# Kernel tuning notes

Hardware: AMD Instinct MI355X
Metric: run time of the kernel (lower is better)

Reference implementation:

```python
import jax, jax.numpy as jnp
import numpy as np

BATCH, SEQ, D_MODEL = 8, 2048, 512
HEADS, BUCKET, N_HASHES = 8, 4, 4
D_HEAD = D_MODEL // HEADS
N_BUCKETS = SEQ // BUCKET
SELF_ATTN_VAL = -5e4  # TOKEN_SELF_ATTN_VALUE in reformer-pytorch


def setup_inputs() -> dict:
    key = jax.random.key(0)
    ks = jax.random.split(key, 8)
    scale = 1.0 / np.sqrt(D_MODEL).astype(np.float32)
    q = jax.random.normal(ks[0], (BATCH, SEQ, D_MODEL), jnp.float32)
    k = jax.random.normal(ks[1], (BATCH, SEQ, D_MODEL), jnp.float32)
    v = jax.random.normal(ks[2], (BATCH, SEQ, D_MODEL), jnp.float32)
    Wqk = jax.random.normal(ks[3], (D_MODEL, D_MODEL), jnp.float32) * scale
    Wv = jax.random.normal(ks[4], (D_MODEL, D_MODEL), jnp.float32) * scale
    Wout = jax.random.normal(ks[5], (D_MODEL, D_MODEL), jnp.float32) * scale
    b_out = jnp.zeros((D_MODEL,), jnp.float32)
    rotations = jax.random.normal(ks[6], (D_HEAD, N_HASHES, N_BUCKETS // 2), jnp.float32)
    return {"queries": q, "keys": k, "values": v, "Wqk": Wqk, "Wv": Wv,
            "Wout": Wout, "b_out": b_out, "rotations": rotations}


def _look_one_back(x):
    # concat each chunk with the previous chunk (wrap-around), along within-chunk axis
    return jnp.concatenate([x, jnp.roll(x, 1, axis=1)], axis=2)


def _lsh_attend(qk, v, rotations, bucket_size, n_hashes):
    # qk, v: (bm, t, d); shared-QK LSH attention (reformer-pytorch defaults)
    bm, t, d = qk.shape
    n_buckets = t // bucket_size
    # --- hash ---
    rotated = jnp.einsum('btf,fhi->bhti', qk, rotations)          # (bm, nh, t, nb/2)
    rotated = jnp.concatenate([rotated, -rotated], axis=-1)       # (bm, nh, t, nb)
    buckets = jnp.argmax(rotated, axis=-1)                        # (bm, nh, t)
    offsets = (jnp.arange(n_hashes) * n_buckets)[None, :, None]
    buckets = (buckets + offsets).reshape(bm, n_hashes * t)
    # --- sort tokens by (bucket, position) ---
    ticker = jnp.arange(n_hashes * t)
    buckets_and_t = t * buckets + (ticker % t)[None, :]           # unique values
    sticker = jnp.argsort(buckets_and_t, axis=-1)                 # (bm, nh*t)
    undo_sort = jnp.argsort(sticker, axis=-1)
    st = sticker % t
    sqk = jnp.take_along_axis(qk, st[:, :, None], axis=1)         # (bm, nh*t, d)
    sv = jnp.take_along_axis(v, st[:, :, None], axis=1)
    # --- chunk ---
    n_chunks = n_hashes * n_buckets
    bq_t = st.reshape(bm, n_chunks, bucket_size)
    bqk = sqk.reshape(bm, n_chunks, bucket_size, d)
    bv = sv.reshape(bm, n_chunks, bucket_size, d)
    bq = bqk
    norm = jnp.maximum(jnp.linalg.norm(bqk, axis=-1, keepdims=True), 1e-12)
    bk = bqk / norm                                               # F.normalize (shared QK)
    bk = _look_one_back(bk)
    bv = _look_one_back(bv)
    bkv_t = jnp.concatenate([bq_t, jnp.roll(bq_t, 1, axis=1)], axis=2)
    # --- attend within chunks ---
    dots = jnp.einsum('bnie,bnje->bnij', bq, bk) * (d ** -0.5)    # (bm, nc, bs, 2bs)
    self_mask = bq_t[:, :, :, None] == bkv_t[:, :, None, :]
    dots = jnp.where(self_mask, SELF_ATTN_VAL, dots)
    dots_lse = jax.nn.logsumexp(dots, axis=-1, keepdims=True)
    probs = jnp.exp(dots - dots_lse)
    bo = jnp.einsum('bnij,bnje->bnie', probs, bv)
    so = bo.reshape(bm, -1, d)
    slogits = dots_lse.reshape(bm, -1)
    # --- unsort and combine hash rounds ---
    o = jnp.take_along_axis(so, undo_sort[:, :, None], axis=1)
    logits = jnp.take_along_axis(slogits, undo_sort, axis=1)
    o = o.reshape(bm, n_hashes, t, d)
    logits = logits.reshape(bm, n_hashes, t, 1)
    w = jnp.exp(logits - jax.nn.logsumexp(logits, axis=1, keepdims=True))
    return jnp.sum(o * w, axis=1)                                 # (bm, t, d)


def reference(queries, keys, values, Wqk, Wv, Wout, b_out, rotations):
    # keys/values are unused by the original module (self-attention on queries)
    B, N, C = queries.shape
    H, d = HEADS, C // HEADS
    qk = jnp.einsum('bnc,cd->bnd', queries, Wqk)
    v = jnp.einsum('bnc,cd->bnd', queries, Wv)
    qk = qk.reshape(B, N, H, d).transpose(0, 2, 1, 3).reshape(B * H, N, d)
    v = v.reshape(B, N, H, d).transpose(0, 2, 1, 3).reshape(B * H, N, d)
    o = _lsh_attend(qk, v, rotations, BUCKET, N_HASHES)
    o = o.reshape(B, H, N, d).transpose(0, 2, 1, 3).reshape(B, N, C)
    return jnp.einsum('bnc,cd->bnd', o, Wout) + b_out
```

## Files before the change

kernel.cpp:

```cpp
#include <hip/hip_runtime.h>
#include <math.h>

#define SELF_VAL (-5e4f)

typedef __attribute__((ext_vector_type(8))) short bf16x8;
typedef __attribute__((ext_vector_type(4))) float f32x4;

__device__ __forceinline__ unsigned short f2bf(float x) {
    unsigned b = __float_as_uint(x);
    b += 0x7FFFu + ((b >> 16) & 1u);
    return (unsigned short)(b >> 16);
}
__device__ __forceinline__ float bf2f(unsigned short h) {
    return __uint_as_float(((unsigned)h) << 16);
}

__global__ __launch_bounds__(256) void k_rotT(const float* __restrict__ rot,
                                              float* __restrict__ rotT2)
{
    int idx = blockIdx.x * 256 + threadIdx.x;
    int h = idx >> 14, k = (idx >> 8) & 63, col = idx & 255;
    rotT2[idx] = rot[k * 1024 + h * 256 + col];
}

__global__ __launch_bounds__(256) void k_woutT(const float* __restrict__ Wout,
                                               unsigned short* __restrict__ WoutT16)
{
    int idx = blockIdx.x * 256 + threadIdx.x;
    int n = idx >> 9, k = idx & 511;
    WoutT16[idx] = f2bf(Wout[(size_t)k * 512 + n]);
}

__global__ __launch_bounds__(256) void k_gemm_qkv(
    const float* __restrict__ Q, const float* __restrict__ Wqk,
    const float* __restrict__ Wv, float* __restrict__ qk, float* __restrict__ vv,
    float* __restrict__ rnorm)
{
    __shared__ float As[16][132];
    __shared__ float Bs[16][132];
    const int bx = blockIdx.x;
    const int mt = bx >> 3, nt = bx & 7;
    const int m0 = mt * 128, n0 = nt * 128;
    const int tid = threadIdx.x;
    const int ty = tid >> 4, tx = tid & 15;
    const float* Bsrc = (n0 < 512) ? (Wqk + n0) : (Wv + (n0 - 512));
    const int ar0 = tid >> 2, acq = (tid & 3) * 4;
    const int ar1 = 64 + (tid >> 2);
    const int bk0 = tid >> 5, bnq = (tid & 31) * 4;
    const int bk1 = 8 + (tid >> 5);
    const float* Aptr0 = Q + (size_t)(m0 + ar0) * 512 + acq;
    const float* Aptr1 = Q + (size_t)(m0 + ar1) * 512 + acq;
    const float* Bptr0 = Bsrc + (size_t)bk0 * 512 + bnq;
    const float* Bptr1 = Bsrc + (size_t)bk1 * 512 + bnq;
    float acc[8][8] = {};
    float4 a0 = *(const float4*)(Aptr0);
    float4 a1 = *(const float4*)(Aptr1);
    float4 b0 = *(const float4*)(Bptr0);
    float4 b1 = *(const float4*)(Bptr1);
    for (int k0 = 0; k0 < 512; k0 += 16) {
        As[acq+0][ar0]=a0.x; As[acq+1][ar0]=a0.y; As[acq+2][ar0]=a0.z; As[acq+3][ar0]=a0.w;
        As[acq+0][ar1]=a1.x; As[acq+1][ar1]=a1.y; As[acq+2][ar1]=a1.z; As[acq+3][ar1]=a1.w;
        *(float4*)&Bs[bk0][bnq] = b0;
        *(float4*)&Bs[bk1][bnq] = b1;
        __syncthreads();
        if (k0 + 16 < 512) {
            a0 = *(const float4*)(Aptr0 + k0 + 16);
            a1 = *(const float4*)(Aptr1 + k0 + 16);
            b0 = *(const float4*)(Bptr0 + (size_t)(k0 + 16) * 512);
            b1 = *(const float4*)(Bptr1 + (size_t)(k0 + 16) * 512);
        }
        #pragma unroll
        for (int kk = 0; kk < 16; kk++) {
            float a_[8], b_[8];
            *(float4*)&a_[0] = *(float4*)&As[kk][ty*4];
            *(float4*)&a_[4] = *(float4*)&As[kk][64 + ty*4];
            *(float4*)&b_[0] = *(float4*)&Bs[kk][tx*4];
            *(float4*)&b_[4] = *(float4*)&Bs[kk][64 + tx*4];
            #pragma unroll
            for (int i = 0; i < 8; i++)
                #pragma unroll
                for (int j = 0; j < 8; j++)
                    acc[i][j] += a_[i] * b_[j];
        }
        __syncthreads();
    }
    #pragma unroll
    for (int ig = 0; ig < 2; ig++) {
        #pragma unroll
        for (int i = 0; i < 4; i++) {
            int row = m0 + ig*64 + ty*4 + i;
            int b = row >> 11, t = row & 2047;
            #pragma unroll
            for (int jg = 0; jg < 2; jg++) {
                int n = n0 + jg*64 + tx*4;
                float4 r4 = make_float4(acc[ig*4+i][jg*4+0], acc[ig*4+i][jg*4+1],
                                        acc[ig*4+i][jg*4+2], acc[ig*4+i][jg*4+3]);
                if (n < 512) {
                    *(float4*)(qk + ((size_t)((b*8 + (n>>6))*2048 + t))*64 + (n&63)) = r4;
                } else {
                    int nv = n - 512;
                    *(float4*)(vv + ((size_t)((b*8 + (nv>>6))*2048 + t))*64 + (nv&63)) = r4;
                }
            }
        }
    }
    if (n0 < 512) {
        #pragma unroll
        for (int jg = 0; jg < 2; jg++) {
            int h = (n0 + jg*64) >> 6;
            #pragma unroll
            for (int ig = 0; ig < 2; ig++) {
                #pragma unroll
                for (int i = 0; i < 4; i++) {
                    float s = acc[ig*4+i][jg*4+0]*acc[ig*4+i][jg*4+0]
                            + acc[ig*4+i][jg*4+1]*acc[ig*4+i][jg*4+1]
                            + acc[ig*4+i][jg*4+2]*acc[ig*4+i][jg*4+2]
                            + acc[ig*4+i][jg*4+3]*acc[ig*4+i][jg*4+3];
                    s += __shfl_xor(s, 1);
                    s += __shfl_xor(s, 2);
                    s += __shfl_xor(s, 4);
                    s += __shfl_xor(s, 8);
                    if (tx == 0) {
                        int row = m0 + ig*64 + ty*4 + i;
                        int b = row >> 11, t = row & 2047;
                        rnorm[((size_t)(b*8 + h))*2048 + t] = 1.0f / fmaxf(sqrtf(s), 1e-12f);
                    }
                }
            }
        }
    }
}

__global__ __launch_bounds__(256) void k_hash(const float* __restrict__ qk,
    const float* __restrict__ rotT2, unsigned* __restrict__ buckets)
{
    __shared__ float As[64*128];
    const int bx = blockIdx.x;
    const int bm = bx >> 4;
    const int row0 = (bx & 15) << 7;
    const int tid = threadIdx.x;
    const int ty = tid >> 4, tx = tid & 15;
    {
        const int r = tid >> 1;
        const int kb = (tid & 1) * 8;
        const float* src = qk + ((size_t)(bm*2048 + row0 + r))*64;
        #pragma unroll
        for (int c = 0; c < 8; c++) {
            float4 a4 = *(const float4*)(src + (size_t)(kb + c)*4);
            int k = (kb + c)*4;
            As[(k+0)*128 + r] = a4.x;
            As[(k+1)*128 + r] = a4.y;
            As[(k+2)*128 + r] = a4.z;
            As[(k+3)*128 + r] = a4.w;
        }
    }
    __syncthreads();
    #pragma unroll 1
    for (int h = 0; h < 4; h++) {
        float bv[8]; unsigned bi[8];
        #pragma unroll
        for (int i = 0; i < 8; i++) { bv[i] = -3.402823466e38f; bi[i] = 0u; }
        #pragma unroll 1
        for (int ch = 0; ch < 4; ch++) {
            const float* bsrc = rotT2 + (size_t)h*16384 + ch*64 + tx*4;
            float acc[8][4] = {};
            #pragma unroll 16
            for (int kk = 0; kk < 64; kk++) {
                float4 b4 = *(const float4*)(bsrc + (size_t)kk*256);
                float a_[8];
                *(float4*)&a_[0] = *(float4*)&As[kk*128 + ty*4];
                *(float4*)&a_[4] = *(float4*)&As[kk*128 + 64 + ty*4];
                float b_[4] = {b4.x, b4.y, b4.z, b4.w};
                #pragma unroll
                for (int i = 0; i < 8; i++)
                    #pragma unroll
                    for (int j = 0; j < 4; j++)
                        acc[i][j] += a_[i] * b_[j];
            }
            #pragma unroll
            for (int j = 0; j < 4; j++) {
                unsigned c0 = (unsigned)(ch*64 + tx*4 + j);
                unsigned nc0 = 256u + c0;
                #pragma unroll
                for (int i = 0; i < 8; i++) {
                    float v = acc[i][j];
                    if (v > bv[i] || (v == bv[i] && c0 < bi[i])) { bv[i] = v; bi[i] = c0; }
                    float nv = -v;
                    if (nv > bv[i] || (nv == bv[i] && nc0 < bi[i])) { bv[i] = nv; bi[i] = nc0; }
                }
            }
        }
        #pragma unroll
        for (int i = 0; i < 8; i++) {
            #pragma unroll
            for (int d = 1; d < 16; d <<= 1) {
                float ov = __shfl_xor(bv[i], d);
                unsigned oi = (unsigned)__shfl_xor((int)bi[i], d);
                if (ov > bv[i] || (ov == bv[i] && oi < bi[i])) { bv[i] = ov; bi[i] = oi; }
            }
        }
        if (tx == 0) {
            #pragma unroll
            for (int i = 0; i < 8; i++) {
                int r = (i < 4) ? (ty*4 + i) : (64 + ty*4 + (i - 4));
                buckets[((size_t)(bm*4 + h))*2048 + row0 + r] = bi[i];
            }
        }
    }
}

__global__ __launch_bounds__(256) void k_sort(const unsigned* __restrict__ buckets,
                                              unsigned* __restrict__ st)
{
    __shared__ unsigned whist[4][512];
    __shared__ unsigned baseb[512];
    const int seg = blockIdx.x;
    const unsigned* bk = buckets + (size_t)seg * 2048;
    unsigned* out = st + (size_t)seg * 2048;
    const int tid = threadIdx.x, w = tid >> 6, lane = tid & 63;
    for (int b = tid; b < 2048; b += 256) ((unsigned*)whist)[b] = 0u;
    __syncthreads();
    unsigned myb[8];
    #pragma unroll
    for (int r = 0; r < 8; r++) {
        int pos = w*512 + r*64 + lane;
        myb[r] = bk[pos];
        atomicAdd(&whist[w][myb[r]], 1u);
    }
    __syncthreads();
    for (int b = tid; b < 512; b += 256) {
        unsigned p = 0;
        #pragma unroll
        for (int ww = 0; ww < 4; ww++) { unsigned t = whist[ww][b]; whist[ww][b] = p; p += t; }
        baseb[b] = p;
    }
    __syncthreads();
    if (tid == 0) {
        unsigned run = 0;
        for (int b = 0; b < 512; b++) { unsigned t = baseb[b]; baseb[b] = run; run += t; }
    }
    __syncthreads();
    for (int b = tid; b < 512; b += 256) {
        unsigned bb = baseb[b];
        #pragma unroll
        for (int ww = 0; ww < 4; ww++) whist[ww][b] += bb;
    }
    __syncthreads();
    for (int r = 0; r < 8; r++) {
        unsigned b = myb[r];
        int pos = w*512 + r*64 + lane;
        unsigned base = whist[w][b];
        unsigned rank = 0;
        for (int j = 0; j < 64; j++) {
            unsigned bj = __shfl(b, j);
            rank += (j < lane && bj == b) ? 1u : 0u;
        }
        out[base + rank] = (unsigned)pos;
        atomicAdd(&whist[w][b], 1u);
    }
}

__global__ __launch_bounds__(256) void k_attn(const float* __restrict__ qk,
    const float* __restrict__ vv, const float* __restrict__ rnorm,
    const unsigned* __restrict__ st, unsigned short* __restrict__ oh16,
    float* __restrict__ logits)
{
    __shared__ float qs[68][68];
    __shared__ float vs[68][68];
    __shared__ unsigned P[68];
    __shared__ float rn[68];
    const int sid = blockIdx.x;
    const int stripi = sid & 31;
    const int seg = sid >> 5;
    const int bm = seg >> 2, h = seg & 3;
    const int G0 = (h*512 + stripi*16) * 4;
    const int tid = threadIdx.x;
    for (int j = tid; j < 68; j += 256) {
        int G = (G0 - 4 + j) & 8191;
        int hg = G >> 11, sg = G & 2047;
        unsigned tok = st[((size_t)(bm*4 + hg))*2048 + sg];
        P[j] = tok;
        rn[j] = rnorm[bm*2048 + (int)tok];
    }
    __syncthreads();
    for (int e = tid; e < 68*16; e += 256) {
        int j = e >> 4, fq = e & 15;
        unsigned tok = P[j];
        size_t base = ((size_t)(bm*2048 + (int)tok))*64 + fq*4;
        *(float4*)&qs[j][fq*4] = *(const float4*)(qk + base);
        *(float4*)&vs[j][fq*4] = *(const float4*)(vv + base);
    }
    __syncthreads();
    const int w = tid >> 6, lane = tid & 63;
    const int half = lane >> 5, qi = (lane >> 3) & 3, jj = lane & 7;
    const int fb = lane & 7;
    for (int cp = 0; cp < 2; cp++) {
        int c = w*4 + cp*2 + half;
        int jq = 4 + c*4 + qi;
        int jk = c*4 + jj;
        float dot = 0.f;
        #pragma unroll
        for (int fq = 0; fq < 16; fq++) {
            float4 q4 = *(float4*)&qs[jq][fq*4];
            float4 k4 = *(float4*)&qs[jk][fq*4];
            dot += q4.x*k4.x + q4.y*k4.y + q4.z*k4.z + q4.w*k4.w;
        }
        dot *= 0.125f * rn[jk];
        if (P[jq] == P[jk]) dot = SELF_VAL;
        float m = dot;
        m = fmaxf(m, __shfl_xor(m, 1));
        m = fmaxf(m, __shfl_xor(m, 2));
        m = fmaxf(m, __shfl_xor(m, 4));
        float ex = expf(dot - m);
        float s = ex;
        s += __shfl_xor(s, 1); s += __shfl_xor(s, 2); s += __shfl_xor(s, 4);
        float lse = m + logf(s);
        float p = expf(dot - lse);
        unsigned tq = P[jq];
        if (jj == 0) logits[((size_t)(bm*4 + h))*2048 + tq] = lse;
        float a0=0,a1=0,a2=0,a3=0,a4a=0,a5=0,a6=0,a7=0;
        #pragma unroll
        for (int j2 = 0; j2 < 8; j2++) {
            float pj = __shfl(p, (lane & 0x38) | j2);
            float4 va = *(float4*)&vs[c*4 + j2][fb*8];
            float4 vb = *(float4*)&vs[c*4 + j2][fb*8 + 4];
            a0 += pj*va.x; a1 += pj*va.y; a2 += pj*va.z; a3 += pj*va.w;
            a4a += pj*vb.x; a5 += pj*vb.y; a6 += pj*vb.z; a7 += pj*vb.w;
        }
        union { unsigned short s[8]; uint4 v; } ob;
        ob.s[0]=f2bf(a0); ob.s[1]=f2bf(a1); ob.s[2]=f2bf(a2); ob.s[3]=f2bf(a3);
        ob.s[4]=f2bf(a4a); ob.s[5]=f2bf(a5); ob.s[6]=f2bf(a6); ob.s[7]=f2bf(a7);
        *(uint4*)(oh16 + ((size_t)((bm*4 + h)*2048 + (int)tq))*64 + fb*8) = ob.v;
    }
}

__global__ __launch_bounds__(256) void k_combine(const unsigned short* __restrict__ oh16,
    const float* __restrict__ logits, unsigned short* __restrict__ comb16)
{
    int w = threadIdx.x >> 6, lane = threadIdx.x & 63;
    int row = blockIdx.x * 4 + w;
    int bm = row >> 11, t = row & 2047;
    int b = bm >> 3, head = bm & 7;
    float l0 = logits[((size_t)(bm*4 + 0))*2048 + t];
    float l1 = logits[((size_t)(bm*4 + 1))*2048 + t];
    float l2 = logits[((size_t)(bm*4 + 2))*2048 + t];
    float l3 = logits[((size_t)(bm*4 + 3))*2048 + t];
    float m = fmaxf(fmaxf(l0, l1), fmaxf(l2, l3));
    float e0 = expf(l0 - m), e1 = expf(l1 - m), e2 = expf(l2 - m), e3 = expf(l3 - m);
    float inv = 1.0f / (e0 + e1 + e2 + e3);
    float o = 0.f;
    o += (e0*inv) * bf2f(oh16[((size_t)((bm*4+0)*2048 + t))*64 + lane]);
    o += (e1*inv) * bf2f(oh16[((size_t)((bm*4+1)*2048 + t))*64 + lane]);
    o += (e2*inv) * bf2f(oh16[((size_t)((bm*4+2)*2048 + t))*64 + lane]);
    o += (e3*inv) * bf2f(oh16[((size_t)((bm*4+3)*2048 + t))*64 + lane]);
    comb16[((size_t)(b*2048 + t))*512 + head*64 + lane] = f2bf(o);
}

__global__ __launch_bounds__(256) void k_gemm_out(
    const unsigned short* __restrict__ comb16, const unsigned short* __restrict__ WoutT16,
    const float* __restrict__ bias, float* __restrict__ out)
{
    __shared__ unsigned short Asl[64*72];
    __shared__ unsigned short Bsl[64*72];
    const int bx = blockIdx.x;
    const int mt = bx >> 3, nt = bx & 7;
    const int m0 = mt*64, n0 = nt*64;
    const int tid = threadIdx.x;
    const int wid = tid >> 6, lane = tid & 63;
    const int wm = wid >> 1, wn = wid & 1;
    const int l15 = lane & 15, l4 = lane >> 4;
    const int srow = tid >> 2, skb = (tid & 3) * 16;
    f32x4 acc[2][2] = {};
    for (int k0 = 0; k0 < 512; k0 += 64) {
        {
            const unsigned short* asrc = comb16 + (size_t)(m0 + srow)*512 + k0 + skb;
            *(uint4*)&Asl[srow*72 + skb]     = *(const uint4*)asrc;
            *(uint4*)&Asl[srow*72 + skb + 8] = *(const uint4*)(asrc + 8);
            const unsigned short* bsrc = WoutT16 + (size_t)(n0 + srow)*512 + k0 + skb;
            *(uint4*)&Bsl[srow*72 + skb]     = *(const uint4*)bsrc;
            *(uint4*)&Bsl[srow*72 + skb + 8] = *(const uint4*)(bsrc + 8);
        }
        __syncthreads();
        #pragma unroll
        for (int kq = 0; kq < 2; kq++) {
            int kb = kq*32 + l4*8;
            bf16x8 a0 = *(bf16x8*)&Asl[(wm*32 +      l15)*72 + kb];
            bf16x8 a1 = *(bf16x8*)&Asl[(wm*32 + 16 + l15)*72 + kb];
            bf16x8 b0 = *(bf16x8*)&Bsl[(wn*32 +      l15)*72 + kb];
            bf16x8 b1 = *(bf16x8*)&Bsl[(wn*32 + 16 + l15)*72 + kb];
            acc[0][0] = __builtin_amdgcn_mfma_f32_16x16x32_bf16(a0, b0, acc[0][0], 0, 0, 0);
            acc[0][1] = __builtin_amdgcn_mfma_f32_16x16x32_bf16(a0, b1, acc[0][1], 0, 0, 0);
            acc[1][0] = __builtin_amdgcn_mfma_f32_16x16x32_bf16(a1, b0, acc[1][0], 0, 0, 0);
            acc[1][1] = __builtin_amdgcn_mfma_f32_16x16x32_bf16(a1, b1, acc[1][1], 0, 0, 0);
        }
        __syncthreads();
    }
    #pragma unroll
    for (int sm = 0; sm < 2; sm++) {
        #pragma unroll
        for (int sn = 0; sn < 2; sn++) {
            int col = n0 + wn*32 + sn*16 + l15;
            float bb = bias[col];
            #pragma unroll
            for (int r = 0; r < 4; r++) {
                int row = m0 + wm*32 + sm*16 + l4*4 + r;
                out[(size_t)row*512 + col] = acc[sm][sn][r] + bb;
            }
        }
    }
}

extern "C" void kernel_launch(void* const* d_in, const int* in_sizes, int n_in,
                              void* d_out, int out_size, void* d_ws, size_t ws_size,
                              hipStream_t stream)
{
    const float* Q    = (const float*)d_in[0];
    const float* Wqk  = (const float*)d_in[3];
    const float* Wv   = (const float*)d_in[4];
    const float* Wout = (const float*)d_in[5];
    const float* bout = (const float*)d_in[6];
    const float* rot  = (const float*)d_in[7];
    float* ws = (float*)d_ws;
    float* qk     = ws;
    float* vv     = ws + 8388608;
    unsigned short* oh16 = (unsigned short*)(ws + 16777216);
    unsigned short* WoutT16 = (unsigned short*)(ws + 33554432);
    unsigned short* comb16  = (unsigned short*)(ws + 50331648);
    float* rnorm  = ws + 58720256;
    float* logits = ws + 58851328;
    unsigned* buckets = (unsigned*)(ws + 59375616);
    unsigned* st      = (unsigned*)(ws + 59899904);
    float* rotT2  = ws + 60424192;
    float* out = (float*)d_out;

    k_rotT    <<<dim3(256),  dim3(256), 0, stream>>>(rot, rotT2);
    k_woutT   <<<dim3(1024), dim3(256), 0, stream>>>(Wout, WoutT16);
    k_gemm_qkv<<<dim3(1024), dim3(256), 0, stream>>>(Q, Wqk, Wv, qk, vv, rnorm);
    k_hash    <<<dim3(1024), dim3(256), 0, stream>>>(qk, rotT2, buckets);
    k_sort    <<<dim3(256),  dim3(256), 0, stream>>>(buckets, st);
    k_attn    <<<dim3(8192), dim3(256), 0, stream>>>(qk, vv, rnorm, st, oh16, logits);
    k_combine <<<dim3(32768),dim3(256), 0, stream>>>(oh16, logits, comb16);
    k_gemm_out<<<dim3(2048), dim3(256), 0, stream>>>(comb16, WoutT16, bout, out);
}
```

Measured before the change: 619.3 us.

## Split QKV GEMM and compute V projection with bf16 MFMA

Splits the fused fp32 QK/V projection into two kernels. QK stays on the fp32 SIMT path, since it feeds hashing and norms that are sensitive to precision. V is computed with bf16 MFMA after converting Q and transposing Wv to bf16. This should cut the V half of the fp32 GEMM cost. In exchange it adds conversion kernels, extra memory traffic and bf16 rounding error in V.

```diff
diff --git a/kernel.cpp b/kernel.cpp
--- a/kernel.cpp
+++ b/kernel.cpp
@@ -31,19 +31,39 @@
     WoutT16[idx] = f2bf(Wout[(size_t)k * 512 + n]);
 }
 
-__global__ __launch_bounds__(256) void k_gemm_qkv(
+__global__ __launch_bounds__(256) void k_wvT(const float* __restrict__ Wv,
+                                             unsigned short* __restrict__ WvT16)
+{
+    int idx = blockIdx.x * 256 + threadIdx.x;
+    int n = idx >> 9, k = idx & 511;
+    WvT16[idx] = f2bf(Wv[(size_t)k * 512 + n]);
+}
+
+__global__ __launch_bounds__(256) void k_q16(const float* __restrict__ Q,
+                                             unsigned short* __restrict__ Q16)
+{
+    int idx = blockIdx.x * 256 + threadIdx.x;
+    const float* src = Q + (size_t)idx * 8;
+    float4 v0 = *(const float4*)src;
+    float4 v1 = *(const float4*)(src + 4);
+    union { unsigned short s[8]; uint4 v; } ob;
+    ob.s[0]=f2bf(v0.x); ob.s[1]=f2bf(v0.y); ob.s[2]=f2bf(v0.z); ob.s[3]=f2bf(v0.w);
+    ob.s[4]=f2bf(v1.x); ob.s[5]=f2bf(v1.y); ob.s[6]=f2bf(v1.z); ob.s[7]=f2bf(v1.w);
+    *(uint4*)(Q16 + (size_t)idx * 8) = ob.v;
+}
+
+__global__ __launch_bounds__(256) void k_gemm_qk(
     const float* __restrict__ Q, const float* __restrict__ Wqk,
-    const float* __restrict__ Wv, float* __restrict__ qk, float* __restrict__ vv,
-    float* __restrict__ rnorm)
+    float* __restrict__ qk, float* __restrict__ rnorm)
 {
     __shared__ float As[16][132];
     __shared__ float Bs[16][132];
     const int bx = blockIdx.x;
-    const int mt = bx >> 3, nt = bx & 7;
+    const int mt = bx >> 2, nt = bx & 3;
     const int m0 = mt * 128, n0 = nt * 128;
     const int tid = threadIdx.x;
     const int ty = tid >> 4, tx = tid & 15;
-    const float* Bsrc = (n0 < 512) ? (Wqk + n0) : (Wv + (n0 - 512));
+    const float* Bsrc = Wqk + n0;
     const int ar0 = tid >> 2, acq = (tid & 3) * 4;
     const int ar1 = 64 + (tid >> 2);
     const int bk0 = tid >> 5, bnq = (tid & 31) * 4;
@@ -95,37 +115,85 @@
                 int n = n0 + jg*64 + tx*4;
                 float4 r4 = make_float4(acc[ig*4+i][jg*4+0], acc[ig*4+i][jg*4+1],
                                         acc[ig*4+i][jg*4+2], acc[ig*4+i][jg*4+3]);
-                if (n < 512) {
-                    *(float4*)(qk + ((size_t)((b*8 + (n>>6))*2048 + t))*64 + (n&63)) = r4;
-                } else {
-                    int nv = n - 512;
-                    *(float4*)(vv + ((size_t)((b*8 + (nv>>6))*2048 + t))*64 + (nv&63)) = r4;
+                *(float4*)(qk + ((size_t)((b*8 + (n>>6))*2048 + t))*64 + (n&63)) = r4;
+            }
+        }
+    }
+    #pragma unroll
+    for (int jg = 0; jg < 2; jg++) {
+        int h = (n0 + jg*64) >> 6;
+        #pragma unroll
+        for (int ig = 0; ig < 2; ig++) {
+            #pragma unroll
+            for (int i = 0; i < 4; i++) {
+                float s = acc[ig*4+i][jg*4+0]*acc[ig*4+i][jg*4+0]
+                        + acc[ig*4+i][jg*4+1]*acc[ig*4+i][jg*4+1]
+                        + acc[ig*4+i][jg*4+2]*acc[ig*4+i][jg*4+2]
+                        + acc[ig*4+i][jg*4+3]*acc[ig*4+i][jg*4+3];
+                s += __shfl_xor(s, 1);
+                s += __shfl_xor(s, 2);
+                s += __shfl_xor(s, 4);
+                s += __shfl_xor(s, 8);
+                if (tx == 0) {
+                    int row = m0 + ig*64 + ty*4 + i;
+                    int b = row >> 11, t = row & 2047;
+                    rnorm[((size_t)(b*8 + h))*2048 + t] = 1.0f / fmaxf(sqrtf(s), 1e-12f);
                 }
             }
         }
     }
-    if (n0 < 512) {
-        #pragma unroll
-        for (int jg = 0; jg < 2; jg++) {
-            int h = (n0 + jg*64) >> 6;
-            #pragma unroll
-            for (int ig = 0; ig < 2; ig++) {
-                #pragma unroll
-                for (int i = 0; i < 4; i++) {
-                    float s = acc[ig*4+i][jg*4+0]*acc[ig*4+i][jg*4+0]
-                            + acc[ig*4+i][jg*4+1]*acc[ig*4+i][jg*4+1]
-                            + acc[ig*4+i][jg*4+2]*acc[ig*4+i][jg*4+2]
-                            + acc[ig*4+i][jg*4+3]*acc[ig*4+i][jg*4+3];
-                    s += __shfl_xor(s, 1);
-                    s += __shfl_xor(s, 2);
-                    s += __shfl_xor(s, 4);
-                    s += __shfl_xor(s, 8);
-                    if (tx == 0) {
-                        int row = m0 + ig*64 + ty*4 + i;
-                        int b = row >> 11, t = row & 2047;
-                        rnorm[((size_t)(b*8 + h))*2048 + t] = 1.0f / fmaxf(sqrtf(s), 1e-12f);
-                    }
-                }
+}
+
+__global__ __launch_bounds__(256) void k_gemm_v(
+    const unsigned short* __restrict__ Q16, const unsigned short* __restrict__ WvT16,
+    float* __restrict__ vv)
+{
+    __shared__ unsigned short Asl[64*72];
+    __shared__ unsigned short Bsl[64*72];
+    const int bx = blockIdx.x;
+    const int mt = bx >> 3, nt = bx & 7;
+    const int m0 = mt*64, n0 = nt*64;
+    const int tid = threadIdx.x;
+    const int wid = tid >> 6, lane = tid & 63;
+    const int wm = wid >> 1, wn = wid & 1;
+    const int l15 = lane & 15, l4 = lane >> 4;
+    const int srow = tid >> 2, skb = (tid & 3) * 16;
+    f32x4 acc[2][2] = {};
+    for (int k0 = 0; k0 < 512; k0 += 64) {
+        {
+            const unsigned short* asrc = Q16 + (size_t)(m0 + srow)*512 + k0 + skb;
+            *(uint4*)&Asl[srow*72 + skb]     = *(const uint4*)asrc;
+            *(uint4*)&Asl[srow*72 + skb + 8] = *(const uint4*)(asrc + 8);
+            const unsigned short* bsrc = WvT16 + (size_t)(n0 + srow)*512 + k0 + skb;
+            *(uint4*)&Bsl[srow*72 + skb]     = *(const uint4*)bsrc;
+            *(uint4*)&Bsl[srow*72 + skb + 8] = *(const uint4*)(bsrc + 8);
+        }
+        __syncthreads();
+        #pragma unroll
+        for (int kq = 0; kq < 2; kq++) {
+            int kb = kq*32 + l4*8;
+            bf16x8 a0 = *(bf16x8*)&Asl[(wm*32 +      l15)*72 + kb];
+            bf16x8 a1 = *(bf16x8*)&Asl[(wm*32 + 16 + l15)*72 + kb];
+            bf16x8 b0 = *(bf16x8*)&Bsl[(wn*32 +      l15)*72 + kb];
+            bf16x8 b1 = *(bf16x8*)&Bsl[(wn*32 + 16 + l15)*72 + kb];
+            acc[0][0] = __builtin_amdgcn_mfma_f32_16x16x32_bf16(a0, b0, acc[0][0], 0, 0, 0);
+            acc[0][1] = __builtin_amdgcn_mfma_f32_16x16x32_bf16(a0, b1, acc[0][1], 0, 0, 0);
+            acc[1][0] = __builtin_amdgcn_mfma_f32_16x16x32_bf16(a1, b0, acc[1][0], 0, 0, 0);
+            acc[1][1] = __builtin_amdgcn_mfma_f32_16x16x32_bf16(a1, b1, acc[1][1], 0, 0, 0);
+        }
+        __syncthreads();
+    }
+    #pragma unroll
+    for (int sm = 0; sm < 2; sm++) {
+        #pragma unroll
+        for (int sn = 0; sn < 2; sn++) {
+            int col = n0 + wn*32 + sn*16 + l15;
+            int h = col >> 6, d = col & 63;
+            #pragma unroll
+            for (int r = 0; r < 4; r++) {
+                int row = m0 + wm*32 + sm*16 + l4*4 + r;
+                int b = row >> 11, t = row & 2047;
+                vv[((size_t)((b*8 + h)*2048 + t))*64 + d] = acc[sm][sn][r];
             }
         }
     }
@@ -425,6 +493,8 @@
     float* vv     = ws + 8388608;
     unsigned short* oh16 = (unsigned short*)(ws + 16777216);
     unsigned short* WoutT16 = (unsigned short*)(ws + 33554432);
+    unsigned short* Q16     = (unsigned short*)(ws + 33685504);
+    unsigned short* WvT16   = (unsigned short*)(ws + 37879808);
     unsigned short* comb16  = (unsigned short*)(ws + 50331648);
     float* rnorm  = ws + 58720256;
     float* logits = ws + 58851328;
@@ -435,7 +505,10 @@
 
     k_rotT    <<<dim3(256),  dim3(256), 0, stream>>>(rot, rotT2);
     k_woutT   <<<dim3(1024), dim3(256), 0, stream>>>(Wout, WoutT16);
-    k_gemm_qkv<<<dim3(1024), dim3(256), 0, stream>>>(Q, Wqk, Wv, qk, vv, rnorm);
+    k_wvT     <<<dim3(1024), dim3(256), 0, stream>>>(Wv, WvT16);
+    k_q16     <<<dim3(4096), dim3(256), 0, stream>>>(Q, Q16);
+    k_gemm_qk <<<dim3(512),  dim3(256), 0, stream>>>(Q, Wqk, qk, rnorm);
+    k_gemm_v  <<<dim3(2048), dim3(256), 0, stream>>>(Q16, WvT16, vv);
     k_hash    <<<dim3(1024), dim3(256), 0, stream>>>(qk, rotT2, buckets);
     k_sort    <<<dim3(256),  dim3(256), 0, stream>>>(buckets, st);
     k_attn    <<<dim3(8192), dim3(256), 0, stream>>>(qk, vv, rnorm, st, oh16, logits);
```

After: 556.6 us, median of 2. -10.1%, faster.
